# Performance work log

Measured on AMD Instinct MI355X. Metric: run time of the kernel, lower is better.

## Reference

```python
import jax, jax.numpy as jnp
import numpy as np
from jax import lax

D = 768
C = 37          # num_classes + 1
PAD_ID = C - 1  # label_init puts '[PAD]' last
B, S = 128, 512


def setup_inputs() -> dict:
    key = jax.random.key(0)
    ks = jax.random.split(key, 8)
    x = jax.random.normal(ks[0], (B, S, D), dtype=jnp.float32)
    W = jax.random.normal(ks[1], (D, C), dtype=jnp.float32) * (1.0 / np.sqrt(D))
    b = jnp.zeros((C,), dtype=jnp.float32)
    start = jax.random.uniform(ks[2], (C,), minval=-0.1, maxval=0.1)
    end = jax.random.uniform(ks[3], (C,), minval=-0.1, maxval=0.1)
    trans = jax.random.uniform(ks[4], (C, C), minval=-0.1, maxval=0.1)
    labels = jax.random.randint(ks[5], (B, S), 0, C)
    lengths = jax.random.randint(ks[6], (B,), 16, S + 1)
    mask = (jnp.arange(S)[None, :] < lengths[:, None])  # first column always True
    return {"x": x, "W": W, "b": b, "start": start, "end": end,
            "trans": trans, "labels": labels, "mask": mask}


def _crf(emissions, labels, mask, start, end, trans):
    # time-major, as in pytorch-crf
    em = jnp.transpose(emissions, (1, 0, 2))      # [S, B, C]
    tg = labels.T                                  # [S, B]
    mkb = mask.T                                   # [S, B] bool
    mkf = mkb.astype(em.dtype)
    bidx = jnp.arange(em.shape[1])

    # ---- gold path score ----
    score0 = start[tg[0]] + em[0, bidx, tg[0]]
    def step_score(carry, inp):
        prev_tag, s = carry
        e_t, t_t, mf, mb = inp
        s = s + (trans[prev_tag, t_t] + e_t[bidx, t_t]) * mf
        prev_tag = jnp.where(mb, t_t, prev_tag)
        return (prev_tag, s), None
    (last_tag, score), _ = lax.scan(step_score, (tg[0], score0),
                                    (em[1:], tg[1:], mkf[1:], mkb[1:]))
    score = score + end[last_tag]

    # ---- log partition (forward algorithm) ----
    alpha0 = start[None, :] + em[0]               # [B, C]
    def step_norm(alpha, inp):
        e_t, mb = inp
        nxt = jax.nn.logsumexp(alpha[:, :, None] + trans[None, :, :], axis=1) + e_t
        return jnp.where(mb[:, None], nxt, alpha), None
    alpha, _ = lax.scan(step_norm, alpha0, (em[1:], mkb[1:]))
    logZ = jax.nn.logsumexp(alpha + end[None, :], axis=1)
    ll = jnp.sum(score - logZ)                    # reduction='sum'

    # ---- Viterbi decode ----
    ident = jnp.arange(C)[None, :]
    v0 = start[None, :] + em[0]
    def step_vit(v, inp):
        e_t, mb = inp
        cand = v[:, :, None] + trans[None, :, :]  # [B, prev, cur]
        bp = jnp.argmax(cand, axis=1)             # [B, C]
        nxt = jnp.max(cand, axis=1) + e_t
        v = jnp.where(mb[:, None], nxt, v)
        bp = jnp.where(mb[:, None], bp, ident)    # identity at padded steps
        return v, bp
    v, bps = lax.scan(step_vit, v0, (em[1:], mkb[1:]))  # bps: [S-1, B, C]
    last = jnp.argmax(v + end[None, :], axis=1)   # [B]
    def back(tag, bp):
        return bp[bidx, tag], tag
    first, rest = lax.scan(back, last, bps, reverse=True)
    tags = jnp.concatenate([first[None, :], rest], axis=0).T  # [B, S]
    tags = jnp.where(mask, tags, PAD_ID)
    return ll, tags


def reference(x, W, b, start, end, trans, labels, mask):
    emissions = jnp.einsum('bsd,dc->bsc', x, W) + b  # linear head
    log_likelihood, tags = _crf(emissions, labels, mask, start, end, trans)
    return log_likelihood, tags
```

## Files before the change

### kernel.cpp

```cpp
#include <hip/hip_runtime.h>

#define Bq 128
#define Sq 512
#define Cq 37
#define Dq 768

typedef __attribute__((ext_vector_type(2))) float f32x2;
typedef __attribute__((ext_vector_type(4))) float f32x4;
typedef __attribute__((ext_vector_type(8))) short bf16x8;

static __device__ __forceinline__ f32x2 pk_fma(f32x2 a, f32x2 b, f32x2 c) {
  f32x2 d; asm("v_pk_fma_f32 %0, %1, %2, %3" : "=v"(d) : "v"(a), "v"(b), "v"(c));
  return d;
}
static __device__ __forceinline__ f32x2 pk_add(f32x2 a, f32x2 b) {
  f32x2 d; asm("v_pk_add_f32 %0, %1, %2" : "=v"(d) : "v"(a), "v"(b));
  return d;
}
static __device__ __forceinline__ float bcast(float v, int p) {
  return __int_as_float(__builtin_amdgcn_ds_bpermute(p << 2, __float_as_int(v)));
}

#define REP18(X) X(0)X(1)X(2)X(3)X(4)X(5)X(6)X(7)X(8)X(9)X(10)X(11)X(12)X(13) \
  X(14)X(15)X(16)X(17)
#define REP37(X) X(0)X(1)X(2)X(3)X(4)X(5)X(6)X(7)X(8)X(9)X(10)X(11)X(12)X(13) \
  X(14)X(15)X(16)X(17)X(18)X(19)X(20)X(21)X(22)X(23)X(24)X(25)X(26)X(27)X(28) \
  X(29)X(30)X(31)X(32)X(33)X(34)X(35)X(36)

#define BR(i) ((((i) & 3) == 0) ? gv[(i) >> 2].x : (((i) & 3) == 1) ? gv[(i) >> 2].y \
             : (((i) & 3) == 2) ? gv[(i) >> 2].z : gv[(i) >> 2].w)

__global__ __launch_bounds__(256) void prep_kernel(
    const float* __restrict__ W, unsigned short* __restrict__ Wbh,
    unsigned short* __restrict__ Wbl)
{
  int i = blockIdx.x * 256 + threadIdx.x;
  if (i >= 24 * 3 * 64 * 8) return;
  int ks = i / 1536, rem = i % 1536;
  int nt = rem / 512, rem2 = rem % 512;
  int lane = rem2 >> 3, j = rem2 & 7;
  int k = ks * 32 + (lane >> 4) * 8 + j;
  int c = nt * 16 + (lane & 15);
  float w = (c < Cq) ? W[(size_t)k * Cq + c] : 0.f;
  unsigned u = __float_as_uint(w);
  unsigned short h = (unsigned short)(u >> 16);
  float hr = __uint_as_float((unsigned)h << 16);
  float r = w - hr;
  Wbh[i] = h;
  Wbl[i] = (unsigned short)(__float_as_uint(r) >> 16);
}

__global__ __launch_bounds__(256) void emis_kernel(
    const float* __restrict__ x, const unsigned short* __restrict__ Wbh,
    const unsigned short* __restrict__ Wbl, const float* __restrict__ bias,
    float* __restrict__ em)
{
  int tid = threadIdx.x, lane = tid & 63;
  int wv = tid >> 6;
  int tokBase = blockIdx.x * 64 + wv * 16;
  int row = lane & 15, kg = lane >> 4;
  const float* xr = x + (size_t)(tokBase + row) * Dq + kg * 8;
  const bf16x8* Bh = (const bf16x8*)Wbh;
  const bf16x8* Bl = (const bf16x8*)Wbl;
  f32x4 acc0 = {0.f, 0.f, 0.f, 0.f};
  f32x4 acc1 = {0.f, 0.f, 0.f, 0.f};
  f32x4 acc2 = {0.f, 0.f, 0.f, 0.f};

  float4 c0 = *(const float4*)(xr);
  float4 c1 = *(const float4*)(xr + 4);
  for (int ks = 0; ks < 24; ++ks) {
    float4 n0, n1;
    if (ks < 23) {
      n0 = *(const float4*)(xr + (ks + 1) * 32);
      n1 = *(const float4*)(xr + (ks + 1) * 32 + 4);
    }
    bf16x8 ah, al;
#define SPLIT(J, V) { unsigned u = __float_as_uint(V); \
    unsigned short h = (unsigned short)(u >> 16); \
    float hr = __uint_as_float((unsigned)h << 16); \
    float rr = (V) - hr; \
    ah[J] = (short)h; al[J] = (short)(__float_as_uint(rr) >> 16); }
    SPLIT(0, c0.x) SPLIT(1, c0.y) SPLIT(2, c0.z) SPLIT(3, c0.w)
    SPLIT(4, c1.x) SPLIT(5, c1.y) SPLIT(6, c1.z) SPLIT(7, c1.w)
#undef SPLIT
    int fi = (ks * 3) * 64 + lane;
    bf16x8 bh0 = Bh[fi], bh1 = Bh[fi + 64], bh2 = Bh[fi + 128];
    bf16x8 bl0 = Bl[fi], bl1 = Bl[fi + 64], bl2 = Bl[fi + 128];
    acc0 = __builtin_amdgcn_mfma_f32_16x16x32_bf16(al, bh0, acc0, 0, 0, 0);
    acc1 = __builtin_amdgcn_mfma_f32_16x16x32_bf16(al, bh1, acc1, 0, 0, 0);
    acc2 = __builtin_amdgcn_mfma_f32_16x16x32_bf16(al, bh2, acc2, 0, 0, 0);
    acc0 = __builtin_amdgcn_mfma_f32_16x16x32_bf16(ah, bl0, acc0, 0, 0, 0);
    acc1 = __builtin_amdgcn_mfma_f32_16x16x32_bf16(ah, bl1, acc1, 0, 0, 0);
    acc2 = __builtin_amdgcn_mfma_f32_16x16x32_bf16(ah, bl2, acc2, 0, 0, 0);
    acc0 = __builtin_amdgcn_mfma_f32_16x16x32_bf16(ah, bh0, acc0, 0, 0, 0);
    acc1 = __builtin_amdgcn_mfma_f32_16x16x32_bf16(ah, bh1, acc1, 0, 0, 0);
    acc2 = __builtin_amdgcn_mfma_f32_16x16x32_bf16(ah, bh2, acc2, 0, 0, 0);
    c0 = n0; c1 = n1;
  }
  int colc = lane & 15;
#pragma unroll
  for (int r = 0; r < 4; ++r) {
    size_t tok = (size_t)tokBase + kg * 4 + r;
    em[tok * Cq + colc]      = acc0[r] + bias[colc];
    em[tok * Cq + 16 + colc] = acc1[r] + bias[16 + colc];
    if (colc < 5)
      em[tok * Cq + 32 + colc] = acc2[r] + bias[32 + colc];
  }
}

__global__ __launch_bounds__(320) void crf_mega_kernel(
    const float* __restrict__ em, const float* __restrict__ startv,
    const float* __restrict__ endv, const float* __restrict__ trans,
    const int* __restrict__ labels, const unsigned char* __restrict__ maskb,
    float* __restrict__ llp, float* __restrict__ outp)
{
  __shared__ float semm[(Sq + 4) * Cq];
  __shared__ float vh[Sq * 40];
  __shared__ __align__(16) float sxA[64];
  __shared__ __align__(16) float sxB[64];
  __shared__ __align__(16) float sxC[64];
  __shared__ __align__(16) float sxD[64];
  __shared__ float mrgA[64], mrgB[64], mrgV[64], mrgU[64];
  __shared__ float s_score;
  __shared__ int s_cstar;
  int b = blockIdx.x;
  int tid = threadIdx.x, wid = tid >> 6, lane = tid & 63;
  int cl = lane < Cq ? lane : Cq - 1;

  int esz4 = (maskb[1] == 0) ? 1 : 0;
  int len = 0;
#pragma unroll
  for (int k = 0; k < 8; ++k) {
    size_t t = (size_t)lane + (size_t)k * 64;
    unsigned char mb = esz4 ? maskb[((size_t)b * Sq + t) * 4] : maskb[(size_t)b * Sq + t];
    len += (mb != 0);
  }
#pragma unroll
  for (int off = 32; off; off >>= 1) len += __shfl_xor(len, off);
  int m = len >> 1;

  const float4* src4 = (const float4*)(em + (size_t)b * Sq * Cq);
  float4* dst4 = (float4*)semm;
  for (int i = tid; i < (Sq * Cq) / 4; i += 320) dst4[i] = src4[i];
  if (tid < 4 * Cq) semm[Sq * Cq + tid] = 0.f;
  __syncthreads();

  const float L2E = 1.4426950408889634f, LN2 = 0.6931471805599453f;

  if (wid == 0) {
    f32x2 E2[18];
#pragma unroll
    for (int i = 0; i < 18; ++i) {
      E2[i][0] = exp2f(trans[(2 * i) * Cq + cl] * L2E);
      E2[i][1] = exp2f(trans[(2 * i + 1) * Cq + cl] * L2E);
    }
    float E36 = exp2f(trans[36 * Cq + cl] * L2E);
    const float4* se4 = (const float4*)sxA;
    float a0 = (lane < Cq) ? (startv[cl] + semm[cl]) : -3.0e38f;
    float K0 = bcast(a0, 0);
    float ez = (lane < Cq) ? exp2f((a0 - K0) * L2E) : 0.f;
    int eacc = 0;
    float wA = exp2f(semm[1 * Cq + cl] * L2E), wB = exp2f(semm[2 * Cq + cl] * L2E);
    float wC = exp2f(semm[3 * Cq + cl] * L2E), wD = exp2f(semm[4 * Cq + cl] * L2E);
    for (int t = 1; t <= m; ++t) {
      sxA[lane] = ez;
      int tn = (t + 4 <= m) ? t + 4 : m;
      float raw = semm[tn * Cq + cl];
      float4 gv[10];
#pragma unroll
      for (int q = 0; q < 10; ++q) gv[q] = se4[q];
      int e0 = ((__float_as_int(gv[0].x) >> 23) & 255) - 127;
      float scale = __int_as_float((127 - e0) << 23);
      f32x2 sa = {0.f, 0.f}, sb2 = {0.f, 0.f};
#define FPK(i) { f32x2 g; \
      g[0] = ((i) & 1) ? gv[(i) >> 1].z : gv[(i) >> 1].x; \
      g[1] = ((i) & 1) ? gv[(i) >> 1].w : gv[(i) >> 1].y; \
      if ((i) & 1) sb2 = pk_fma(g, E2[i], sb2); else sa = pk_fma(g, E2[i], sa); }
      REP18(FPK)
#undef FPK
      float dot = ((sa[0] + sb2[0]) + (sa[1] + sb2[1])) + gv[9].x * E36;
      float wcur = wA; wA = wB; wB = wC; wC = wD;
      ez = dot * (wcur * scale);
      eacc += e0;
      wD = exp2f(raw * L2E);
    }
    mrgA[lane] = (lane < Cq) ? LN2 * (log2f(ez) + (float)eacc) + K0 : -3.0e38f;
  } else if (wid == 1) {
    f32x2 E2[18];
#pragma unroll
    for (int i = 0; i < 18; ++i) {
      E2[i][0] = exp2f(trans[cl * Cq + 2 * i] * L2E);
      E2[i][1] = exp2f(trans[cl * Cq + 2 * i + 1] * L2E);
    }
    float E36 = exp2f(trans[cl * Cq + 36] * L2E);
    const float4* se4 = (const float4*)sxB;
    float b0v = (lane < Cq) ? endv[cl] : -3.0e38f;
    float KB = bcast(b0v, 0);
    float bz = (lane < Cq) ? exp2f((b0v - KB) * L2E) : 0.f;
    int eacc = 0;
    float wA = exp2f(semm[(len - 1) * Cq + cl] * L2E);
    float wB = exp2f(semm[(len - 2) * Cq + cl] * L2E);
    float wC = exp2f(semm[(len - 3) * Cq + cl] * L2E);
    float wD = exp2f(semm[(len - 4) * Cq + cl] * L2E);
    for (int t = len - 2; t >= m; --t) {
      float wcur = wA; wA = wB; wB = wC; wC = wD;
      float s = bz * wcur;
      sxB[lane] = s;
      int tn = (t - 3 > 0) ? t - 3 : 0;
      float raw = semm[tn * Cq + cl];
      float4 gv[10];
#pragma unroll
      for (int q = 0; q < 10; ++q) gv[q] = se4[q];
      int e0 = ((__float_as_int(gv[0].x) >> 23) & 255) - 127;
      float scale = __int_as_float((127 - e0) << 23);
      f32x2 sa = {0.f, 0.f}, sb2 = {0.f, 0.f};
#define FPK(i) { f32x2 g; \
      g[0] = ((i) & 1) ? gv[(i) >> 1].z : gv[(i) >> 1].x; \
      g[1] = ((i) & 1) ? gv[(i) >> 1].w : gv[(i) >> 1].y; \
      if ((i) & 1) sb2 = pk_fma(g, E2[i], sb2); else sa = pk_fma(g, E2[i], sa); }
      REP18(FPK)
#undef FPK
      float dot = ((sa[0] + sb2[0]) + (sa[1] + sb2[1])) + gv[9].x * E36;
      bz = dot * scale;
      eacc += e0;
      wD = exp2f(raw * L2E);
    }
    mrgB[lane] = (lane < Cq) ? LN2 * (log2f(bz) + (float)eacc) + KB : -3.0e38f;
  } else if (wid == 2) {
    f32x2 T2[18];
#pragma unroll
    for (int i = 0; i < 18; ++i) {
      T2[i][0] = trans[(2 * i) * Cq + cl];
      T2[i][1] = trans[(2 * i + 1) * Cq + cl];
    }
    float T36 = trans[36 * Cq + cl];
    const float4* sv4 = (const float4*)sxC;
    float v = (lane < Cq) ? (startv[cl] + semm[cl]) : -3.0e38f;
    if (lane < 40) vh[0 * 40 + lane] = v;
    float emA = semm[1 * Cq + cl], emB = semm[2 * Cq + cl];
    float emC = semm[3 * Cq + cl], emD = semm[4 * Cq + cl];
    for (int t = 1; t <= m; ++t) {
      sxC[lane] = v;
      int tn = (t + 4 <= m) ? t + 4 : m;
      float raw = semm[tn * Cq + cl];
      float4 gv[10];
#pragma unroll
      for (int q = 0; q < 10; ++q) gv[q] = sv4[q];
      float m0 = -3.0e38f, m1 = -3.0e38f, m2 = -3.0e38f, m3 = -3.0e38f;
#define VPK(i) { f32x2 g; \
      g[0] = ((i) & 1) ? gv[(i) >> 1].z : gv[(i) >> 1].x; \
      g[1] = ((i) & 1) ? gv[(i) >> 1].w : gv[(i) >> 1].y; \
      f32x2 c = pk_add(g, T2[i]); \
      if (((i) & 3) == 0) m0 = fmaxf(fmaxf(m0, c[0]), c[1]); \
      else if (((i) & 3) == 1) m1 = fmaxf(fmaxf(m1, c[0]), c[1]); \
      else if (((i) & 3) == 2) m2 = fmaxf(fmaxf(m2, c[0]), c[1]); \
      else m3 = fmaxf(fmaxf(m3, c[0]), c[1]); }
      REP18(VPK)
#undef VPK
      float c36 = gv[9].x + T36;
      float best = fmaxf(fmaxf(fmaxf(m0, m1), fmaxf(m2, m3)), c36);
      float emc = emA; emA = emB; emB = emC; emC = emD;
      v = (lane < Cq) ? best + emc : -3.0e38f;
      if (lane < 40) vh[t * 40 + lane] = v;
      emD = raw;
    }
    mrgV[lane] = v;
  } else if (wid == 3) {
    f32x2 T2[18];
#pragma unroll
    for (int i = 0; i < 18; ++i) {
      T2[i][0] = trans[cl * Cq + 2 * i];
      T2[i][1] = trans[cl * Cq + 2 * i + 1];
    }
    float T36 = trans[cl * Cq + 36];
    const float4* sv4 = (const float4*)sxD;
    float u = (lane < Cq) ? endv[cl] : -3.0e38f;
    float emA = semm[(len - 1) * Cq + cl], emB = semm[(len - 2) * Cq + cl];
    float emC = semm[(len - 3) * Cq + cl], emD = semm[(len - 4) * Cq + cl];
    for (int t = len - 2; t >= m; --t) {
      float emc = emA; emA = emB; emB = emC; emC = emD;
      float s = u + emc;
      sxD[lane] = s;
      if (lane < 40) vh[(t + 1) * 40 + lane] = (lane < Cq) ? s : -3.0e38f;
      int tn = (t - 3 > 0) ? t - 3 : 0;
      float raw = semm[tn * Cq + cl];
      float4 gv[10];
#pragma unroll
      for (int q = 0; q < 10; ++q) gv[q] = sv4[q];
      float m0 = -3.0e38f, m1 = -3.0e38f, m2 = -3.0e38f, m3 = -3.0e38f;
#define VPK(i) { f32x2 g; \
      g[0] = ((i) & 1) ? gv[(i) >> 1].z : gv[(i) >> 1].x; \
      g[1] = ((i) & 1) ? gv[(i) >> 1].w : gv[(i) >> 1].y; \
      f32x2 c = pk_add(g, T2[i]); \
      if (((i) & 3) == 0) m0 = fmaxf(fmaxf(m0, c[0]), c[1]); \
      else if (((i) & 3) == 1) m1 = fmaxf(fmaxf(m1, c[0]), c[1]); \
      else if (((i) & 3) == 2) m2 = fmaxf(fmaxf(m2, c[0]), c[1]); \
      else m3 = fmaxf(fmaxf(m3, c[0]), c[1]); }
      REP18(VPK)
#undef VPK
      float c36 = gv[9].x + T36;
      float best = fmaxf(fmaxf(fmaxf(m0, m1), fmaxf(m2, m3)), c36);
      u = (lane < Cq) ? best : -3.0e38f;
      emD = raw;
    }
    mrgU[lane] = u;
  } else {
    const int* lab = labels + (size_t)b * Sq;
    float sc = 0.f;
#pragma unroll
    for (int k = 0; k < 8; ++k) {
      int t = 1 + lane + k * 64;
      if (t < len) {
        int lp = lab[t - 1], lt = lab[t];
        sc += trans[lp * Cq + lt] + semm[t * Cq + lt];
      }
    }
#pragma unroll
    for (int off = 32; off; off >>= 1) sc += __shfl_xor(sc, off);
    if (lane == 0) {
      int l0 = lab[0], lf = lab[len - 1];
      s_score = sc + startv[l0] + semm[l0] + endv[lf];
    }
  }
  __syncthreads();

  unsigned char* bpl = (unsigned char*)semm;
  if (wid == 0) {
    float xv = (lane < Cq) ? mrgA[lane] + mrgB[lane] : -3.0e38f;
    float mm = xv;
#pragma unroll
    for (int off = 32; off; off >>= 1) mm = fmaxf(mm, __shfl_xor(mm, off));
    float es = exp2f((xv - mm) * L2E);
#pragma unroll
    for (int off = 32; off; off >>= 1) es += __shfl_xor(es, off);
    float logZ = mm + log2f(es) * LN2;
    float pv = (lane < Cq) ? mrgV[lane] + mrgU[lane] : -3.0e38f;
    int idx = (lane < Cq) ? lane : 1000;
#pragma unroll
    for (int off = 32; off; off >>= 1) {
      float po = __shfl_xor(pv, off); int io = __shfl_xor(idx, off);
      if (po > pv || (po == pv && io < idx)) { pv = po; idx = io; }
    }
    if (lane == 0) { llp[b] = s_score - logZ; s_cstar = idx; }
  } else if (wid <= 2) {
#define DT(i) float T##i = trans[(i) * Cq + cl];
    REP37(DT)
#undef DT
    for (int t = wid; t <= m; t += 2) {
      const float4* vr4 = (const float4*)&vh[(t - 1) * 40];
      float4 gv[10];
#pragma unroll
      for (int q = 0; q < 10; ++q) gv[q] = vr4[q];
      float best = -3.0e38f; int bi = 0;
#define BARG(i) { float cnd = BR(i) + T##i; if (cnd > best) { best = cnd; bi = (i); } }
      REP37(BARG)
#undef BARG
      if (lane < Cq) bpl[cl * 520 + t] = (unsigned char)bi;
    }
  } else {
#define DR(i) float R##i = trans[cl * Cq + (i)];
    REP37(DR)
#undef DR
    for (int s = m + 1 + (wid - 3); s < len; s += 2) {
      const float4* vr4 = (const float4*)&vh[s * 40];
      float4 gv[10];
#pragma unroll
      for (int q = 0; q < 10; ++q) gv[q] = vr4[q];
      float best = -3.0e38f; int bi = 0;
#define BARG(i) { float cnd = BR(i) + R##i; if (cnd > best) { best = cnd; bi = (i); } }
      REP37(BARG)
#undef BARG
      if (lane < Cq) bpl[cl * 520 + s] = (unsigned char)bi;
    }
  }
  __syncthreads();

  if (wid == 0) {
    int cstar = __builtin_amdgcn_readfirstlane(s_cstar);
    int lenv = __builtin_amdgcn_readfirstlane(len);
    int mv = __builtin_amdgcn_readfirstlane(m);
    int rowc = lane < Cq ? lane : Cq - 1;
    const unsigned* rw = (const unsigned*)(bpl + rowc * 520);
    unsigned r[128];
#pragma unroll
    for (int k = 0; k < 128; ++k) r[k] = rw[k];
    unsigned vt[8];
#pragma unroll
    for (int j = 0; j < 8; ++j) vt[j] = 0u;
#pragma unroll
    for (int j = 0; j < 8; ++j)
      vt[j] = (lane == (mv & 63) && (mv >> 6) == j) ? (unsigned)cstar : vt[j];
    {
      int tag = cstar;
#pragma unroll
      for (int t = 1; t <= 510; ++t) {
        int word = __builtin_amdgcn_readlane((int)r[t >> 2], tag);
        int nt = (word >> ((t & 3) * 8)) & 0xff;
        bool live = (t > mv) && (t < lenv);
        tag = live ? nt : tag;
        vt[t >> 6] = (lane == (t & 63) && live) ? (unsigned)tag : vt[t >> 6];
      }
    }
    {
      int tag = cstar;
#pragma unroll
      for (int t = 510; t >= 0; --t) {
        int word = __builtin_amdgcn_readlane((int)r[(t + 1) >> 2], tag);
        int nt = (word >> (((t + 1) & 3) * 8)) & 0xff;
        bool live = (t + 1 <= mv);
        tag = live ? nt : tag;
        vt[t >> 6] = (lane == (t & 63) && live) ? (unsigned)tag : vt[t >> 6];
      }
    }
#pragma unroll
    for (int j = 0; j < 8; ++j) {
      int t = j * 64 + lane;
      float o = (t < lenv) ? (float)(int)vt[j] : 36.0f;
      outp[(size_t)b * Sq + t] = o;
    }
  }
}

__global__ __launch_bounds__(64) void ll_reduce_kernel(
    const float* __restrict__ llp, float* __restrict__ outp)
{
  int lane = threadIdx.x;
  float s = llp[lane] + llp[lane + 64];
#pragma unroll
  for (int off = 32; off; off >>= 1) s += __shfl_xor(s, off);
  if (lane == 0) outp[0] = s;
}

extern "C" void kernel_launch(void* const* d_in, const int* in_sizes, int n_in,
                              void* d_out, int out_size, void* d_ws, size_t ws_size,
                              hipStream_t stream)
{
  const float* x      = (const float*)d_in[0];
  const float* W      = (const float*)d_in[1];
  const float* bias   = (const float*)d_in[2];
  const float* startv = (const float*)d_in[3];
  const float* endv   = (const float*)d_in[4];
  const float* trans  = (const float*)d_in[5];
  const int*   labels = (const int*)d_in[6];
  const unsigned char* maskb = (const unsigned char*)d_in[7];
  float* out = (float*)d_out;

  char* ws = (char*)d_ws;
  float* em            = (float*)(ws);
  float* llp           = (float*)(ws + 9699328);
  unsigned short* Wbh  = (unsigned short*)(ws + 9699840);
  unsigned short* Wbl  = (unsigned short*)(ws + 9773568);

  prep_kernel<<<144, 256, 0, stream>>>(W, Wbh, Wbl);
  emis_kernel<<<1024, 256, 0, stream>>>(x, Wbh, Wbl, bias, em);
  crf_mega_kernel<<<128, 320, 0, stream>>>(em, startv, endv, trans, labels, maskb,
                                           llp, out + 1);
  ll_reduce_kernel<<<1, 64, 0, stream>>>(llp, out);
}
```

Measured before the change: 198.5 us.

## Split Viterbi backtrace into separate kernel via global backpointer buffer

```diff
diff --git a/kernel.cpp b/kernel.cpp
--- a/kernel.cpp
+++ b/kernel.cpp
@@ -4,6 +4,7 @@
 #define Sq 512
 #define Cq 37
 #define Dq 768
+#define VST 40
 
 typedef __attribute__((ext_vector_type(2))) float f32x2;
 typedef __attribute__((ext_vector_type(4))) float f32x4;
@@ -112,7 +113,8 @@
     const float* __restrict__ em, const float* __restrict__ startv,
     const float* __restrict__ endv, const float* __restrict__ trans,
     const int* __restrict__ labels, const unsigned char* __restrict__ maskb,
-    float* __restrict__ llp, float* __restrict__ outp)
+    float* __restrict__ llp, unsigned char* __restrict__ bp,
+    int* __restrict__ lenp, int* __restrict__ lastp, int* __restrict__ midp)
 {
   __shared__ float semm[(Sq + 4) * Cq];
   __shared__ float vh[Sq * 40];
@@ -122,7 +124,6 @@
   __shared__ __align__(16) float sxD[64];
   __shared__ float mrgA[64], mrgB[64], mrgV[64], mrgU[64];
   __shared__ float s_score;
-  __shared__ int s_cstar;
   int b = blockIdx.x;
   int tid = threadIdx.x, wid = tid >> 6, lane = tid & 63;
   int cl = lane < Cq ? lane : Cq - 1;
@@ -324,7 +325,6 @@
   }
   __syncthreads();
 
-  unsigned char* bpl = (unsigned char*)semm;
   if (wid == 0) {
     float xv = (lane < Cq) ? mrgA[lane] + mrgB[lane] : -3.0e38f;
     float mm = xv;
@@ -341,7 +341,10 @@
       float po = __shfl_xor(pv, off); int io = __shfl_xor(idx, off);
       if (po > pv || (po == pv && io < idx)) { pv = po; idx = io; }
     }
-    if (lane == 0) { llp[b] = s_score - logZ; s_cstar = idx; }
+    if (lane == 0) {
+      llp[b] = s_score - logZ;
+      lastp[b] = idx; lenp[b] = len; midp[b] = m;
+    }
   } else if (wid <= 2) {
 #define DT(i) float T##i = trans[(i) * Cq + cl];
     REP37(DT)
@@ -355,7 +358,7 @@
 #define BARG(i) { float cnd = BR(i) + T##i; if (cnd > best) { best = cnd; bi = (i); } }
       REP37(BARG)
 #undef BARG
-      if (lane < Cq) bpl[cl * 520 + t] = (unsigned char)bi;
+      if (lane < Cq) bp[((size_t)b * VST + cl) * Sq + t] = (unsigned char)bi;
     }
   } else {
 #define DR(i) float R##i = trans[cl * Cq + (i)];
@@ -370,54 +373,61 @@
 #define BARG(i) { float cnd = BR(i) + R##i; if (cnd > best) { best = cnd; bi = (i); } }
       REP37(BARG)
 #undef BARG
-      if (lane < Cq) bpl[cl * 520 + s] = (unsigned char)bi;
-    }
-  }
-  __syncthreads();
-
-  if (wid == 0) {
-    int cstar = __builtin_amdgcn_readfirstlane(s_cstar);
-    int lenv = __builtin_amdgcn_readfirstlane(len);
-    int mv = __builtin_amdgcn_readfirstlane(m);
-    int rowc = lane < Cq ? lane : Cq - 1;
-    const unsigned* rw = (const unsigned*)(bpl + rowc * 520);
-    unsigned r[128];
-#pragma unroll
-    for (int k = 0; k < 128; ++k) r[k] = rw[k];
-    unsigned vt[8];
-#pragma unroll
-    for (int j = 0; j < 8; ++j) vt[j] = 0u;
-#pragma unroll
-    for (int j = 0; j < 8; ++j)
-      vt[j] = (lane == (mv & 63) && (mv >> 6) == j) ? (unsigned)cstar : vt[j];
-    {
-      int tag = cstar;
-#pragma unroll
-      for (int t = 1; t <= 510; ++t) {
-        int word = __builtin_amdgcn_readlane((int)r[t >> 2], tag);
-        int nt = (word >> ((t & 3) * 8)) & 0xff;
-        bool live = (t > mv) && (t < lenv);
-        tag = live ? nt : tag;
-        vt[t >> 6] = (lane == (t & 63) && live) ? (unsigned)tag : vt[t >> 6];
-      }
-    }
-    {
-      int tag = cstar;
-#pragma unroll
-      for (int t = 510; t >= 0; --t) {
-        int word = __builtin_amdgcn_readlane((int)r[(t + 1) >> 2], tag);
-        int nt = (word >> (((t + 1) & 3) * 8)) & 0xff;
-        bool live = (t + 1 <= mv);
-        tag = live ? nt : tag;
-        vt[t >> 6] = (lane == (t & 63) && live) ? (unsigned)tag : vt[t >> 6];
-      }
-    }
-#pragma unroll
-    for (int j = 0; j < 8; ++j) {
-      int t = j * 64 + lane;
-      float o = (t < lenv) ? (float)(int)vt[j] : 36.0f;
-      outp[(size_t)b * Sq + t] = o;
-    }
+      if (lane < Cq) bp[((size_t)b * VST + cl) * Sq + s] = (unsigned char)bi;
+    }
+  }
+}
+
+__global__ __launch_bounds__(64) void crf_back_kernel(
+    const unsigned char* __restrict__ bp, const int* __restrict__ lenp,
+    const int* __restrict__ lastp, const int* __restrict__ midp,
+    float* __restrict__ outp)
+{
+  int b = blockIdx.x, lane = threadIdx.x;
+  int len = __builtin_amdgcn_readfirstlane(lenp[b]);
+  int m = __builtin_amdgcn_readfirstlane(midp[b]);
+  int cstar = __builtin_amdgcn_readfirstlane(lastp[b]);
+  int row = lane < VST ? lane : VST - 1;
+  const uint4* src = (const uint4*)(bp + ((size_t)b * VST + row) * Sq);
+  unsigned r[128];
+#pragma unroll
+  for (int k = 0; k < 32; ++k) {
+    uint4 q = src[k];
+    r[4 * k] = q.x; r[4 * k + 1] = q.y; r[4 * k + 2] = q.z; r[4 * k + 3] = q.w;
+  }
+  unsigned vt[8];
+#pragma unroll
+  for (int j = 0; j < 8; ++j) vt[j] = 0u;
+#pragma unroll
+  for (int j = 0; j < 8; ++j)
+    vt[j] = (lane == (m & 63) && (m >> 6) == j) ? (unsigned)cstar : vt[j];
+  {
+    int tag = cstar;
+#pragma unroll
+    for (int t = 1; t <= 510; ++t) {
+      int word = __builtin_amdgcn_readlane((int)r[t >> 2], tag);
+      int nt = (word >> ((t & 3) * 8)) & 0xff;
+      bool live = (t > m) && (t < len);
+      tag = live ? nt : tag;
+      vt[t >> 6] = (lane == (t & 63) && live) ? (unsigned)tag : vt[t >> 6];
+    }
+  }
+  {
+    int tag = cstar;
+#pragma unroll
+    for (int t = 510; t >= 0; --t) {
+      int word = __builtin_amdgcn_readlane((int)r[(t + 1) >> 2], tag);
+      int nt = (word >> (((t + 1) & 3) * 8)) & 0xff;
+      bool live = (t + 1 <= m);
+      tag = live ? nt : tag;
+      vt[t >> 6] = (lane == (t & 63) && live) ? (unsigned)tag : vt[t >> 6];
+    }
+  }
+#pragma unroll
+  for (int j = 0; j < 8; ++j) {
+    int t = j * 64 + lane;
+    float o = (t < len) ? (float)(int)vt[j] : 36.0f;
+    outp[(size_t)b * Sq + t] = o;
   }
 }
 
@@ -448,12 +458,17 @@
   char* ws = (char*)d_ws;
   float* em            = (float*)(ws);
   float* llp           = (float*)(ws + 9699328);
-  unsigned short* Wbh  = (unsigned short*)(ws + 9699840);
-  unsigned short* Wbl  = (unsigned short*)(ws + 9773568);
+  int*   lenp          = (int*)(ws + 9699840);
+  int*   lastp         = (int*)(ws + 9700352);
+  int*   midp          = (int*)(ws + 9700864);
+  unsigned short* Wbh  = (unsigned short*)(ws + 9701376);
+  unsigned short* Wbl  = (unsigned short*)(ws + 9775104);
+  unsigned char* bpbuf = (unsigned char*)(ws + 9848832);
 
   prep_kernel<<<144, 256, 0, stream>>>(W, Wbh, Wbl);
   emis_kernel<<<1024, 256, 0, stream>>>(x, Wbh, Wbl, bias, em);
   crf_mega_kernel<<<128, 320, 0, stream>>>(em, startv, endv, trans, labels, maskb,
-                                           llp, out + 1);
+                                           llp, bpbuf, lenp, lastp, midp);
+  crf_back_kernel<<<128, 64, 0, stream>>>(bpbuf, lenp, lastp, midp, out + 1);
   ll_reduce_kernel<<<1, 64, 0, stream>>>(llp, out);
 }
```

Measured after the change: 203.5 us. 2.6% more time.
